# Performance work log

Measured on AMD Instinct MI355X. Metric: run time of the kernel, lower is better.

Reference implementation:

```python
import jax, jax.numpy as jnp
import numpy as np

L, B, T, C, H, V = 8, 8, 1024, 768, 12, 1024
D = C // H  # head dim 64
FF = 4 * C
EPS = 1e-5


def _ln(h, g, b):
    mu = jnp.mean(h, axis=-1, keepdims=True)
    var = jnp.mean((h - mu) ** 2, axis=-1, keepdims=True)
    return (h - mu) * jax.lax.rsqrt(var + EPS) * g + b


def _ffn(h, W1, b1, W2, b2):
    return jax.nn.gelu(h @ W1 + b1, approximate=False) @ W2 + b2


def setup_inputs() -> dict:
    key = jax.random.key(0)
    ks = jax.random.split(key, 16)
    s = 0.02
    inp = {
        "x": jax.random.randint(ks[0], (B, T), 0, V),
        "embed": jax.random.normal(ks[1], (V, C), jnp.float32) * s,
        "pos": jax.random.normal(ks[2], (T, C), jnp.float32) * s,
        "Wqkv": jax.random.normal(ks[3], (L, C, 3 * C), jnp.float32) * s,
        "bqkv": jnp.zeros((L, 3 * C), jnp.float32),
        "W1a": jax.random.normal(ks[4], (L, C, FF), jnp.float32) * s,
        "b1a": jnp.zeros((L, FF), jnp.float32),
        "W2a": jax.random.normal(ks[5], (L, FF, C), jnp.float32) * s,
        "b2a": jnp.zeros((L, C), jnp.float32),
        "g1": jnp.ones((L, C), jnp.float32),
        "beta1": jnp.zeros((L, C), jnp.float32),
        "W1b": jax.random.normal(ks[6], (L, C, FF), jnp.float32) * s,
        "b1b": jnp.zeros((L, FF), jnp.float32),
        "W2b": jax.random.normal(ks[7], (L, FF, C), jnp.float32) * s,
        "b2b": jnp.zeros((L, C), jnp.float32),
        "g2": jnp.ones((L, C), jnp.float32),
        "beta2": jnp.zeros((L, C), jnp.float32),
        "lm_W": jax.random.normal(ks[8], (C, V), jnp.float32) * s,
        "lm_b": jnp.zeros((V,), jnp.float32),
    }
    return inp


def reference(x, embed, pos, Wqkv, bqkv, W1a, b1a, W2a, b2a, g1, beta1,
              W1b, b1b, W2b, b2b, g2, beta2, lm_W, lm_b):
    h = embed[x] + pos[:T]  # (B,T,C)
    causal = jnp.tril(jnp.ones((T, T), bool))

    def block(h, p):
        (Wqkv, bqkv, W1a, b1a, W2a, b2a, g1, beta1,
         W1b, b1b, W2b, b2b, g2, beta2) = p
        qkv = h @ Wqkv + bqkv  # (B,T,3C); split order is K,Q,V per source
        K, Q, Vv = jnp.split(qkv, 3, axis=-1)
        K = K.reshape(B, T, H, D).transpose(0, 2, 1, 3)
        Q = Q.reshape(B, T, H, D).transpose(0, 2, 1, 3)
        Vv = Vv.reshape(B, T, H, D).transpose(0, 2, 1, 3)
        att = jnp.einsum("bhqd,bhkd->bhqk", Q, K) / jnp.sqrt(jnp.float32(D))
        att = jnp.where(causal, att, -jnp.inf)
        att = jax.nn.softmax(att, axis=-1)
        y = jnp.einsum("bhqk,bhkd->bhqd", att, Vv)
        y = y.transpose(0, 2, 1, 3).reshape(B, T, C)
        y = _ffn(y, W1a, b1a, W2a, b2a)  # FFN inside SelfAttn
        h = h + _ln(y, g1, beta1)        # post-norm residual, as in source
        h = h + _ln(_ffn(h, W1b, b1b, W2b, b2b), g2, beta2)
        return h, None

    params = (Wqkv, bqkv, W1a, b1a, W2a, b2a, g1, beta1,
              W1b, b1b, W2b, b2b, g2, beta2)
    h, _ = jax.lax.scan(block, h, params)
    return h @ lm_W + lm_b  # (B,T,V) logits
```

## Files before the change

### kernel.cpp

```cpp
#include <hip/hip_runtime.h>
#include <hip/hip_bf16.h>

#define L_ 8
#define B_ 8
#define T_ 1024
#define C_ 768
#define H_ 12
#define D_HEAD 64
#define V_ 1024
#define FF_ 3072
#define M_ (B_ * T_)

typedef __bf16 bf16x8 __attribute__((ext_vector_type(8)));
typedef float f32x4 __attribute__((ext_vector_type(4)));

typedef const __attribute__((address_space(1))) void* as1cvp;
typedef __attribute__((address_space(3))) void* as3vp;

__device__ __forceinline__ void async16(const void* g, void* l) {
  __builtin_amdgcn_global_load_lds((as1cvp)g, (as3vp)l, 16, 0, 0);
}

__device__ __forceinline__ float bf2f(unsigned short u) {
  union { unsigned u32; float f; } c; c.u32 = ((unsigned)u) << 16; return c.f;
}

__device__ __forceinline__ unsigned short f2bf(float f) {
  __hip_bfloat16 h = __float2bfloat16(f);
  return *(unsigned short*)&h;
}

__device__ __forceinline__ float gelu_f(float x) {
  return 0.5f * x * (1.0f + erff(x * 0.70710678118654752f));
}

__global__ __launch_bounds__(256) void embed_kernel(
    const int* __restrict__ x, const float* __restrict__ emb,
    const float* __restrict__ pos, float* __restrict__ h,
    __hip_bfloat16* __restrict__ hb) {
  int row = blockIdx.x;
  int t = row & (T_ - 1);
  int id = x[row];
#pragma unroll
  for (int j = 0; j < 3; ++j) {
    int c = threadIdx.x + j * 256;
    float v = emb[(size_t)id * C_ + c] + pos[(size_t)t * C_ + c];
    h[(size_t)row * C_ + c] = v;
    hb[(size_t)row * C_ + c] = __float2bfloat16(v);
  }
}

__global__ void transpose_cast(const float* __restrict__ W,
                               __hip_bfloat16* __restrict__ Wt, int K, int N) {
  __shared__ float tile[32][33];
  int nb = blockIdx.x * 32, kb = blockIdx.y * 32;
  int tx = threadIdx.x, ty = threadIdx.y;
#pragma unroll
  for (int r = 0; r < 4; ++r)
    tile[ty + r * 8][tx] = W[(size_t)(kb + ty + r * 8) * N + nb + tx];
  __syncthreads();
#pragma unroll
  for (int r = 0; r < 4; ++r)
    Wt[(size_t)(nb + ty + r * 8) * K + kb + tx] =
        __float2bfloat16(tile[tx][ty + r * 8]);
}

__global__ void transpose_cast2(const float* __restrict__ Wa,
                                __hip_bfloat16* __restrict__ Wta,
                                const float* __restrict__ Wb,
                                __hip_bfloat16* __restrict__ Wtb, int K, int N) {
  __shared__ float tile[32][33];
  const float* W = blockIdx.z ? Wb : Wa;
  __hip_bfloat16* Wt = blockIdx.z ? Wtb : Wta;
  int nb = blockIdx.x * 32, kb = blockIdx.y * 32;
  int tx = threadIdx.x, ty = threadIdx.y;
#pragma unroll
  for (int r = 0; r < 4; ++r)
    tile[ty + r * 8][tx] = W[(size_t)(kb + ty + r * 8) * N + nb + tx];
  __syncthreads();
#pragma unroll
  for (int r = 0; r < 4; ++r)
    Wt[(size_t)(nb + ty + r * 8) * K + kb + tx] =
        __float2bfloat16(tile[tx][ty + r * 8]);
}

template <int ACT_GELU, int OUT_BF16>
__global__ __launch_bounds__(256, 2) void gemm_bt(
    const __hip_bfloat16* __restrict__ A, const __hip_bfloat16* __restrict__ Bt,
    const float* __restrict__ bias, void* __restrict__ Cv, int M, int N, int K) {
  __shared__ __align__(16) __hip_bfloat16 As[128 * 32];
  __shared__ __align__(16) __hip_bfloat16 Bs[128 * 32];
  const int tid = threadIdx.x;
  const int lane = tid & 63, wv = tid >> 6;
  const int lane4 = lane & 15, quad = lane >> 4;
  const int wr = wv >> 1, wc = wv & 1;
  const int bm = blockIdx.y * 128, bn = blockIdx.x * 128;

  const int r0 = tid >> 2, kc0 = (tid & 3) * 8;
  const __hip_bfloat16* gA0 = A + (size_t)(bm + r0) * K + kc0;
  const __hip_bfloat16* gA1 = gA0 + (size_t)64 * K;
  const __hip_bfloat16* gB0 = Bt + (size_t)(bn + r0) * K + kc0;
  const __hip_bfloat16* gB1 = gB0 + (size_t)64 * K;
  __hip_bfloat16* lA0 = As + tid * 8;
  __hip_bfloat16* lA1 = As + (tid + 256) * 8;
  __hip_bfloat16* lB0 = Bs + tid * 8;
  __hip_bfloat16* lB1 = Bs + (tid + 256) * 8;

  f32x4 acc[4][4] = {};

  for (int k0 = 0; k0 < K; k0 += 32) {
    async16(gA0 + k0, lA0);
    async16(gA1 + k0, lA1);
    async16(gB0 + k0, lB0);
    async16(gB1 + k0, lB1);
    __syncthreads();
    bf16x8 af[4], bfv[4];
#pragma unroll
    for (int i = 0; i < 4; ++i)
      af[i] = *(const bf16x8*)(As + (wr * 64 + i * 16 + lane4) * 32 + quad * 8);
#pragma unroll
    for (int j = 0; j < 4; ++j)
      bfv[j] = *(const bf16x8*)(Bs + (wc * 64 + j * 16 + lane4) * 32 + quad * 8);
#pragma unroll
    for (int i = 0; i < 4; ++i)
#pragma unroll
      for (int j = 0; j < 4; ++j)
        acc[i][j] = __builtin_amdgcn_mfma_f32_16x16x32_bf16(af[i], bfv[j],
                                                            acc[i][j], 0, 0, 0);
    __syncthreads();
  }

#pragma unroll
  for (int i = 0; i < 4; ++i) {
    int row0 = bm + wr * 64 + i * 16 + quad * 4;
#pragma unroll
    for (int j = 0; j < 4; ++j) {
      int col = bn + wc * 64 + j * 16 + lane4;
      float bv = bias[col];
#pragma unroll
      for (int r = 0; r < 4; ++r) {
        float v = acc[i][j][r] + bv;
        if (ACT_GELU) v = gelu_f(v);
        size_t off = (size_t)(row0 + r) * N + col;
        if (OUT_BF16)
          ((__hip_bfloat16*)Cv)[off] = __float2bfloat16(v);
        else
          ((float*)Cv)[off] = v;
      }
    }
  }
}

__global__ __launch_bounds__(256) void attn_mfma(
    const __hip_bfloat16* __restrict__ qkv, __hip_bfloat16* __restrict__ y) {
  __shared__ __align__(16) __hip_bfloat16 VtS[64][72];
  __shared__ __align__(16) __hip_bfloat16 Ps[4][16][72];

  const int tid = threadIdx.x;
  const int lane = tid & 63, w = tid >> 6;
  const int lane4 = lane & 15, quad = lane >> 4;
  const int qt = gridDim.x - 1 - blockIdx.x;
  const int bh = blockIdx.y;
  const int b = bh / H_, hh = bh % H_;
  const unsigned short* qk16 = (const unsigned short*)qkv;
  const size_t base = (size_t)b * T_ * (3 * C_) + hh * D_HEAD;

  union FragU { bf16x8 v; unsigned short s[8]; uint4 q; };

  FragU aq[2];
  {
    const unsigned short* qp =
        qk16 + base + (size_t)(qt * 64 + w * 16 + lane4) * (3 * C_) + C_ +
        quad * 8;
#pragma unroll
    for (int c = 0; c < 2; ++c) {
      FragU t;
      t.q = *(const uint4*)(qp + c * 32);
#pragma unroll
      for (int j = 0; j < 8; ++j) aq[c].s[j] = f2bf(bf2f(t.s[j]) * 0.125f);
    }
  }

  const unsigned short* kbase0 =
      qk16 + base + (size_t)(lane4)*(3 * C_) + quad * 8;
  const unsigned short* vbase =
      qk16 + base + (size_t)lane * (3 * C_) + 2 * C_ + w * 16;
  const size_t tile_stride = (size_t)64 * (3 * C_);

  f32x4 o_acc[4] = {};
  float m_r[4] = {-1e30f, -1e30f, -1e30f, -1e30f};
  float l_r[4] = {0.f, 0.f, 0.f, 0.f};

  FragU kc[4][2];
  uint4 vc0, vc1;
  {
    const unsigned short* kp = kbase0;
#pragma unroll
    for (int nt = 0; nt < 4; ++nt) {
      kc[nt][0].q = *(const uint4*)(kp + nt * 16 * (3 * C_));
      kc[nt][1].q = *(const uint4*)(kp + nt * 16 * (3 * C_) + 32);
    }
    vc0 = *(const uint4*)vbase;
    vc1 = *(const uint4*)(vbase + 8);
  }

  for (int kt = 0; kt <= qt; ++kt) {
    FragU kn[4][2];
    uint4 vn0, vn1;
    {
      int ktn = (kt < qt) ? kt + 1 : qt;
      const unsigned short* kp = kbase0 + (size_t)ktn * tile_stride;
#pragma unroll
      for (int nt = 0; nt < 4; ++nt) {
        kn[nt][0].q = *(const uint4*)(kp + nt * 16 * (3 * C_));
        kn[nt][1].q = *(const uint4*)(kp + nt * 16 * (3 * C_) + 32);
      }
      const unsigned short* vp = vbase + (size_t)ktn * tile_stride;
      vn0 = *(const uint4*)vp;
      vn1 = *(const uint4*)(vp + 8);
    }

    f32x4 s_acc[4] = {};
#pragma unroll
    for (int nt = 0; nt < 4; ++nt) {
      s_acc[nt] = __builtin_amdgcn_mfma_f32_16x16x32_bf16(aq[0].v, kc[nt][0].v,
                                                          s_acc[nt], 0, 0, 0);
      s_acc[nt] = __builtin_amdgcn_mfma_f32_16x16x32_bf16(aq[1].v, kc[nt][1].v,
                                                          s_acc[nt], 0, 0, 0);
    }

    if (kt == qt) {
      int qloc = w * 16 + quad * 4;
#pragma unroll
      for (int nt = 0; nt < 4; ++nt) {
        int kloc = nt * 16 + lane4;
#pragma unroll
        for (int r = 0; r < 4; ++r)
          if (kloc > qloc + r) s_acc[nt][r] = -1e30f;
      }
    }

    float p[4][4], alpha[4], ts[4];
#pragma unroll
    for (int r = 0; r < 4; ++r) {
      float tm = fmaxf(fmaxf(s_acc[0][r], s_acc[1][r]),
                       fmaxf(s_acc[2][r], s_acc[3][r]));
      tm = fmaxf(tm, __shfl_xor(tm, 1));
      tm = fmaxf(tm, __shfl_xor(tm, 2));
      tm = fmaxf(tm, __shfl_xor(tm, 4));
      tm = fmaxf(tm, __shfl_xor(tm, 8));
      float mn = fmaxf(m_r[r], tm);
      alpha[r] = __expf(m_r[r] - mn);
      m_r[r] = mn;
      float sr = 0.f;
#pragma unroll
      for (int nt = 0; nt < 4; ++nt) {
        float pv = __expf(s_acc[nt][r] - mn);
        p[nt][r] = pv;
        sr += pv;
      }
      sr += __shfl_xor(sr, 1);
      sr += __shfl_xor(sr, 2);
      sr += __shfl_xor(sr, 4);
      sr += __shfl_xor(sr, 8);
      ts[r] = sr;
    }
#pragma unroll
    for (int r = 0; r < 4; ++r) {
      l_r[r] = l_r[r] * alpha[r] + ts[r];
#pragma unroll
      for (int nt = 0; nt < 4; ++nt) o_acc[nt][r] *= alpha[r];
    }

    __syncthreads();

    {
      const unsigned short* vs = (const unsigned short*)&vc0;
#pragma unroll
      for (int j = 0; j < 8; ++j)
        *(unsigned short*)&VtS[w * 16 + j][lane] = vs[j];
      vs = (const unsigned short*)&vc1;
#pragma unroll
      for (int j = 0; j < 8; ++j)
        *(unsigned short*)&VtS[w * 16 + 8 + j][lane] = vs[j];
    }
#pragma unroll
    for (int nt = 0; nt < 4; ++nt)
#pragma unroll
      for (int r = 0; r < 4; ++r)
        *(unsigned short*)&Ps[w][quad * 4 + r][nt * 16 + lane4] =
            f2bf(p[nt][r]);

    __syncthreads();

    FragU ap0, ap1;
    ap0.v = *(const bf16x8*)&Ps[w][lane4][quad * 8];
    ap1.v = *(const bf16x8*)&Ps[w][lane4][32 + quad * 8];
#pragma unroll
    for (int nt = 0; nt < 4; ++nt) {
      bf16x8 bv0 = *(const bf16x8*)&VtS[nt * 16 + lane4][quad * 8];
      bf16x8 bv1 = *(const bf16x8*)&VtS[nt * 16 + lane4][32 + quad * 8];
      o_acc[nt] = __builtin_amdgcn_mfma_f32_16x16x32_bf16(ap0.v, bv0,
                                                          o_acc[nt], 0, 0, 0);
      o_acc[nt] = __builtin_amdgcn_mfma_f32_16x16x32_bf16(ap1.v, bv1,
                                                          o_acc[nt], 0, 0, 0);
    }

#pragma unroll
    for (int nt = 0; nt < 4; ++nt) {
      kc[nt][0] = kn[nt][0];
      kc[nt][1] = kn[nt][1];
    }
    vc0 = vn0;
    vc1 = vn1;
  }

  float inv[4];
#pragma unroll
  for (int r = 0; r < 4; ++r) inv[r] = 1.f / l_r[r];
#pragma unroll
  for (int nt = 0; nt < 4; ++nt) {
#pragma unroll
    for (int r = 0; r < 4; ++r) {
      int row = qt * 64 + w * 16 + quad * 4 + r;
      __hip_bfloat16* yp =
          y + (size_t)(b * T_ + row) * C_ + hh * D_HEAD + nt * 16 + lane4;
      *yp = __float2bfloat16(o_acc[nt][r] * inv[r]);
    }
  }
}

__global__ __launch_bounds__(256) void resid_ln(
    float* __restrict__ h, const float* __restrict__ z,
    const float* __restrict__ g, const float* __restrict__ be,
    __hip_bfloat16* __restrict__ hb) {
  int row = blockIdx.x;
  int tid = threadIdx.x;
  const float* zr = z + (size_t)row * C_;
  float v[3], s = 0.f, s2 = 0.f;
#pragma unroll
  for (int j = 0; j < 3; ++j) {
    v[j] = zr[tid + 256 * j];
    s += v[j];
    s2 += v[j] * v[j];
  }
#pragma unroll
  for (int msk = 1; msk < 64; msk <<= 1) {
    s += __shfl_xor(s, msk);
    s2 += __shfl_xor(s2, msk);
  }
  __shared__ float red[8];
  int w = tid >> 6;
  if ((tid & 63) == 0) { red[w] = s; red[4 + w] = s2; }
  __syncthreads();
  s = red[0] + red[1] + red[2] + red[3];
  s2 = red[4] + red[5] + red[6] + red[7];
  float mu = s * (1.f / C_);
  float var = s2 * (1.f / C_) - mu * mu;
  float rstd = rsqrtf(var + 1e-5f);
  float* hr = h + (size_t)row * C_;
  __hip_bfloat16* hbr = hb + (size_t)row * C_;
#pragma unroll
  for (int j = 0; j < 3; ++j) {
    int c = tid + 256 * j;
    float nv = hr[c] + (v[j] - mu) * rstd * g[c] + be[c];
    hr[c] = nv;
    hbr[c] = __float2bfloat16(nv);
  }
}

extern "C" void kernel_launch(void* const* d_in, const int* in_sizes, int n_in,
                              void* d_out, int out_size, void* d_ws,
                              size_t ws_size, hipStream_t stream) {
  const int* x = (const int*)d_in[0];
  const float* embed = (const float*)d_in[1];
  const float* pos = (const float*)d_in[2];
  const float* Wqkv = (const float*)d_in[3];
  const float* bqkv = (const float*)d_in[4];
  const float* W1a = (const float*)d_in[5];
  const float* b1a = (const float*)d_in[6];
  const float* W2a = (const float*)d_in[7];
  const float* b2a = (const float*)d_in[8];
  const float* g1 = (const float*)d_in[9];
  const float* be1 = (const float*)d_in[10];
  const float* W1b = (const float*)d_in[11];
  const float* b1b = (const float*)d_in[12];
  const float* W2b = (const float*)d_in[13];
  const float* b2b = (const float*)d_in[14];
  const float* g2 = (const float*)d_in[15];
  const float* be2 = (const float*)d_in[16];
  const float* lmW = (const float*)d_in[17];
  const float* lmb = (const float*)d_in[18];
  float* out = (float*)d_out;

  char* p = (char*)d_ws;
  auto alloc = [&](size_t bytes) {
    void* r = (void*)p;
    p += (bytes + 255) & ~(size_t)255;
    return r;
  };
  float* h = (float*)alloc((size_t)M_ * C_ * 4);
  __hip_bfloat16* hb = (__hip_bfloat16*)alloc((size_t)M_ * C_ * 2);
  __hip_bfloat16* qkv = (__hip_bfloat16*)alloc((size_t)M_ * 3 * C_ * 2);
  __hip_bfloat16* ybuf = (__hip_bfloat16*)alloc((size_t)M_ * C_ * 2);
  __hip_bfloat16* ubuf = (__hip_bfloat16*)alloc((size_t)M_ * FF_ * 2);
  float* zbuf = (float*)alloc((size_t)M_ * C_ * 4);
  __hip_bfloat16* Wtqkv = (__hip_bfloat16*)alloc((size_t)(3 * C_) * C_ * 2);
  __hip_bfloat16* Wt1a = (__hip_bfloat16*)alloc((size_t)FF_ * C_ * 2);
  __hip_bfloat16* Wt1b = (__hip_bfloat16*)alloc((size_t)FF_ * C_ * 2);
  __hip_bfloat16* Wt2a = (__hip_bfloat16*)alloc((size_t)C_ * FF_ * 2);
  __hip_bfloat16* Wt2b = (__hip_bfloat16*)alloc((size_t)C_ * FF_ * 2);

  dim3 blk256(256);
  embed_kernel<<<M_, blk256, 0, stream>>>(x, embed, pos, h, hb);

  for (int l = 0; l < L_; ++l) {
    transpose_cast<<<dim3(3 * C_ / 32, C_ / 32), dim3(32, 8), 0, stream>>>(
        Wqkv + (size_t)l * C_ * 3 * C_, Wtqkv, C_, 3 * C_);
    transpose_cast2<<<dim3(FF_ / 32, C_ / 32, 2), dim3(32, 8), 0, stream>>>(
        W1a + (size_t)l * C_ * FF_, Wt1a, W1b + (size_t)l * C_ * FF_, Wt1b,
        C_, FF_);
    transpose_cast2<<<dim3(C_ / 32, FF_ / 32, 2), dim3(32, 8), 0, stream>>>(
        W2a + (size_t)l * FF_ * C_, Wt2a, W2b + (size_t)l * FF_ * C_, Wt2b,
        FF_, C_);

    gemm_bt<0, 1><<<dim3(3 * C_ / 128, M_ / 128), blk256, 0, stream>>>(
        hb, Wtqkv, bqkv + (size_t)l * 3 * C_, qkv, M_, 3 * C_, C_);
    attn_mfma<<<dim3(T_ / 64, B_ * H_), blk256, 0, stream>>>(qkv, ybuf);
    gemm_bt<1, 1><<<dim3(FF_ / 128, M_ / 128), blk256, 0, stream>>>(
        ybuf, Wt1a, b1a + (size_t)l * FF_, ubuf, M_, FF_, C_);
    gemm_bt<0, 0><<<dim3(C_ / 128, M_ / 128), blk256, 0, stream>>>(
        ubuf, Wt2a, b2a + (size_t)l * C_, zbuf, M_, C_, FF_);
    resid_ln<<<M_, blk256, 0, stream>>>(h, zbuf, g1 + (size_t)l * C_,
                                        be1 + (size_t)l * C_, hb);
    gemm_bt<1, 1><<<dim3(FF_ / 128, M_ / 128), blk256, 0, stream>>>(
        hb, Wt1b, b1b + (size_t)l * FF_, ubuf, M_, FF_, C_);
    gemm_bt<0, 0><<<dim3(C_ / 128, M_ / 128), blk256, 0, stream>>>(
        ubuf, Wt2b, b2b + (size_t)l * C_, zbuf, M_, C_, FF_);
    resid_ln<<<M_, blk256, 0, stream>>>(h, zbuf, g2 + (size_t)l * C_,
                                        be2 + (size_t)l * C_, hb);
  }

  transpose_cast<<<dim3(V_ / 32, C_ / 32), dim3(32, 8), 0, stream>>>(
      lmW, Wtqkv, C_, V_);
  gemm_bt<0, 0><<<dim3(V_ / 128, M_ / 128), blk256, 0, stream>>>(
      hb, Wtqkv, lmb, out, M_, V_, C_);
}
```

Before: 4.149 ms.

## Pair causal attention query tiles per block and transpose MFMA operands

```diff
diff --git a/kernel.cpp b/kernel.cpp
--- a/kernel.cpp
+++ b/kernel.cpp
@@ -153,179 +153,182 @@
 
 __global__ __launch_bounds__(256) void attn_mfma(
     const __hip_bfloat16* __restrict__ qkv, __hip_bfloat16* __restrict__ y) {
-  __shared__ __align__(16) __hip_bfloat16 VtS[64][72];
-  __shared__ __align__(16) __hip_bfloat16 Ps[4][16][72];
+  __shared__ __align__(16) __hip_bfloat16 VtS[2][64][72];
+  __shared__ __align__(16) __hip_bfloat16 Ps[2][4][16][72];
 
   const int tid = threadIdx.x;
   const int lane = tid & 63, w = tid >> 6;
   const int lane4 = lane & 15, quad = lane >> 4;
-  const int qt = gridDim.x - 1 - blockIdx.x;
   const int bh = blockIdx.y;
   const int b = bh / H_, hh = bh % H_;
   const unsigned short* qk16 = (const unsigned short*)qkv;
   const size_t base = (size_t)b * T_ * (3 * C_) + hh * D_HEAD;
+  const size_t tile_stride = (size_t)64 * (3 * C_);
+  const int NTILE = T_ / 64;
 
   union FragU { bf16x8 v; unsigned short s[8]; uint4 q; };
 
-  FragU aq[2];
-  {
-    const unsigned short* qp =
-        qk16 + base + (size_t)(qt * 64 + w * 16 + lane4) * (3 * C_) + C_ +
-        quad * 8;
-#pragma unroll
-    for (int c = 0; c < 2; ++c) {
-      FragU t;
-      t.q = *(const uint4*)(qp + c * 32);
-#pragma unroll
-      for (int j = 0; j < 8; ++j) aq[c].s[j] = f2bf(bf2f(t.s[j]) * 0.125f);
-    }
-  }
-
   const unsigned short* kbase0 =
-      qk16 + base + (size_t)(lane4)*(3 * C_) + quad * 8;
+      qk16 + base + (size_t)lane4 * (3 * C_) + quad * 8;
   const unsigned short* vbase =
       qk16 + base + (size_t)lane * (3 * C_) + 2 * C_ + w * 16;
-  const size_t tile_stride = (size_t)64 * (3 * C_);
-
-  f32x4 o_acc[4] = {};
-  float m_r[4] = {-1e30f, -1e30f, -1e30f, -1e30f};
-  float l_r[4] = {0.f, 0.f, 0.f, 0.f};
-
-  FragU kc[4][2];
-  uint4 vc0, vc1;
-  {
-    const unsigned short* kp = kbase0;
-#pragma unroll
-    for (int nt = 0; nt < 4; ++nt) {
-      kc[nt][0].q = *(const uint4*)(kp + nt * 16 * (3 * C_));
-      kc[nt][1].q = *(const uint4*)(kp + nt * 16 * (3 * C_) + 32);
+
+  int buf = 0;
+
+  for (int qi = 0; qi < 2; ++qi) {
+    const int qt = qi ? blockIdx.x : (NTILE - 1 - blockIdx.x);
+
+    FragU aq[2];
+    {
+      const unsigned short* qp =
+          qk16 + base + (size_t)(qt * 64 + w * 16 + lane4) * (3 * C_) + C_ +
+          quad * 8;
+#pragma unroll
+      for (int c = 0; c < 2; ++c) {
+        FragU t;
+        t.q = *(const uint4*)(qp + c * 32);
+#pragma unroll
+        for (int j = 0; j < 8; ++j) aq[c].s[j] = f2bf(bf2f(t.s[j]) * 0.125f);
+      }
     }
-    vc0 = *(const uint4*)vbase;
-    vc1 = *(const uint4*)(vbase + 8);
-  }
-
-  for (int kt = 0; kt <= qt; ++kt) {
-    FragU kn[4][2];
-    uint4 vn0, vn1;
+
+    f32x4 o_acc[4] = {};
+    float m_r = -1e30f, l_r = 0.f;
+
+    FragU kc[4][2];
+    uint4 vc0, vc1;
     {
-      int ktn = (kt < qt) ? kt + 1 : qt;
-      const unsigned short* kp = kbase0 + (size_t)ktn * tile_stride;
+      const unsigned short* kp = kbase0;
 #pragma unroll
       for (int nt = 0; nt < 4; ++nt) {
-        kn[nt][0].q = *(const uint4*)(kp + nt * 16 * (3 * C_));
-        kn[nt][1].q = *(const uint4*)(kp + nt * 16 * (3 * C_) + 32);
-      }
-      const unsigned short* vp = vbase + (size_t)ktn * tile_stride;
-      vn0 = *(const uint4*)vp;
-      vn1 = *(const uint4*)(vp + 8);
+        kc[nt][0].q = *(const uint4*)(kp + nt * 16 * (3 * C_));
+        kc[nt][1].q = *(const uint4*)(kp + nt * 16 * (3 * C_) + 32);
+      }
+      vc0 = *(const uint4*)vbase;
+      vc1 = *(const uint4*)(vbase + 8);
     }
 
-    f32x4 s_acc[4] = {};
-#pragma unroll
-    for (int nt = 0; nt < 4; ++nt) {
-      s_acc[nt] = __builtin_amdgcn_mfma_f32_16x16x32_bf16(aq[0].v, kc[nt][0].v,
-                                                          s_acc[nt], 0, 0, 0);
-      s_acc[nt] = __builtin_amdgcn_mfma_f32_16x16x32_bf16(aq[1].v, kc[nt][1].v,
-                                                          s_acc[nt], 0, 0, 0);
+    for (int kt = 0; kt <= qt; ++kt) {
+      FragU kn[4][2];
+      uint4 vn0, vn1;
+      {
+        int ktn = (kt < qt) ? kt + 1 : qt;
+        const unsigned short* kp = kbase0 + (size_t)ktn * tile_stride;
+#pragma unroll
+        for (int nt = 0; nt < 4; ++nt) {
+          kn[nt][0].q = *(const uint4*)(kp + nt * 16 * (3 * C_));
+          kn[nt][1].q = *(const uint4*)(kp + nt * 16 * (3 * C_) + 32);
+        }
+        const unsigned short* vp = vbase + (size_t)ktn * tile_stride;
+        vn0 = *(const uint4*)vp;
+        vn1 = *(const uint4*)(vp + 8);
+      }
+
+      f32x4 s_acc[4] = {};
+#pragma unroll
+      for (int nt = 0; nt < 4; ++nt) {
+        s_acc[nt] = __builtin_amdgcn_mfma_f32_16x16x32_bf16(
+            kc[nt][0].v, aq[0].v, s_acc[nt], 0, 0, 0);
+        s_acc[nt] = __builtin_amdgcn_mfma_f32_16x16x32_bf16(
+            kc[nt][1].v, aq[1].v, s_acc[nt], 0, 0, 0);
+      }
+
+      if (kt == qt) {
+        int qloc = w * 16 + lane4;
+#pragma unroll
+        for (int nt = 0; nt < 4; ++nt) {
+          int k0loc = nt * 16 + quad * 4;
+#pragma unroll
+          for (int r = 0; r < 4; ++r)
+            if (k0loc + r > qloc) s_acc[nt][r] = -1e30f;
+        }
+      }
+
+      float a0 = fmaxf(fmaxf(s_acc[0][0], s_acc[0][1]),
+                       fmaxf(s_acc[0][2], s_acc[0][3]));
+      float a1 = fmaxf(fmaxf(s_acc[1][0], s_acc[1][1]),
+                       fmaxf(s_acc[1][2], s_acc[1][3]));
+      float a2 = fmaxf(fmaxf(s_acc[2][0], s_acc[2][1]),
+                       fmaxf(s_acc[2][2], s_acc[2][3]));
+      float a3 = fmaxf(fmaxf(s_acc[3][0], s_acc[3][1]),
+                       fmaxf(s_acc[3][2], s_acc[3][3]));
+      float tm = fmaxf(fmaxf(a0, a1), fmaxf(a2, a3));
+      tm = fmaxf(tm, __shfl_xor(tm, 16));
+      tm = fmaxf(tm, __shfl_xor(tm, 32));
+      float mn = fmaxf(m_r, tm);
+      float alpha = __expf(m_r - mn);
+      m_r = mn;
+
+      float sr = 0.f;
+#pragma unroll
+      for (int nt = 0; nt < 4; ++nt) {
+        float p0 = __expf(s_acc[nt][0] - mn);
+        float p1 = __expf(s_acc[nt][1] - mn);
+        float p2 = __expf(s_acc[nt][2] - mn);
+        float p3 = __expf(s_acc[nt][3] - mn);
+        sr += (p0 + p1) + (p2 + p3);
+        union { unsigned short s[4]; uint2 u; } pk;
+        pk.s[0] = f2bf(p0);
+        pk.s[1] = f2bf(p1);
+        pk.s[2] = f2bf(p2);
+        pk.s[3] = f2bf(p3);
+        *(uint2*)&Ps[buf][w][lane4][nt * 16 + quad * 4] = pk.u;
+      }
+      sr += __shfl_xor(sr, 16);
+      sr += __shfl_xor(sr, 32);
+      l_r = l_r * alpha + sr;
+
+#pragma unroll
+      for (int dt = 0; dt < 4; ++dt)
+#pragma unroll
+        for (int r = 0; r < 4; ++r) o_acc[dt][r] *= alpha;
+
+      {
+        const unsigned short* vs = (const unsigned short*)&vc0;
+#pragma unroll
+        for (int j = 0; j < 8; ++j)
+          *(unsigned short*)&VtS[buf][w * 16 + j][lane] = vs[j];
+        vs = (const unsigned short*)&vc1;
+#pragma unroll
+        for (int j = 0; j < 8; ++j)
+          *(unsigned short*)&VtS[buf][w * 16 + 8 + j][lane] = vs[j];
+      }
+
+      __syncthreads();
+
+      FragU pp0, pp1;
+      pp0.v = *(const bf16x8*)&Ps[buf][w][lane4][quad * 8];
+      pp1.v = *(const bf16x8*)&Ps[buf][w][lane4][32 + quad * 8];
+#pragma unroll
+      for (int dt = 0; dt < 4; ++dt) {
+        bf16x8 bv0 = *(const bf16x8*)&VtS[buf][dt * 16 + lane4][quad * 8];
+        bf16x8 bv1 = *(const bf16x8*)&VtS[buf][dt * 16 + lane4][32 + quad * 8];
+        o_acc[dt] = __builtin_amdgcn_mfma_f32_16x16x32_bf16(bv0, pp0.v,
+                                                            o_acc[dt], 0, 0, 0);
+        o_acc[dt] = __builtin_amdgcn_mfma_f32_16x16x32_bf16(bv1, pp1.v,
+                                                            o_acc[dt], 0, 0, 0);
+      }
+
+#pragma unroll
+      for (int nt = 0; nt < 4; ++nt) {
+        kc[nt][0] = kn[nt][0];
+        kc[nt][1] = kn[nt][1];
+      }
+      vc0 = vn0;
+      vc1 = vn1;
+      buf ^= 1;
     }
 
-    if (kt == qt) {
-      int qloc = w * 16 + quad * 4;
-#pragma unroll
-      for (int nt = 0; nt < 4; ++nt) {
-        int kloc = nt * 16 + lane4;
-#pragma unroll
-        for (int r = 0; r < 4; ++r)
-          if (kloc > qloc + r) s_acc[nt][r] = -1e30f;
-      }
-    }
-
-    float p[4][4], alpha[4], ts[4];
-#pragma unroll
-    for (int r = 0; r < 4; ++r) {
-      float tm = fmaxf(fmaxf(s_acc[0][r], s_acc[1][r]),
-                       fmaxf(s_acc[2][r], s_acc[3][r]));
-      tm = fmaxf(tm, __shfl_xor(tm, 1));
-      tm = fmaxf(tm, __shfl_xor(tm, 2));
-      tm = fmaxf(tm, __shfl_xor(tm, 4));
-      tm = fmaxf(tm, __shfl_xor(tm, 8));
-      float mn = fmaxf(m_r[r], tm);
-      alpha[r] = __expf(m_r[r] - mn);
-      m_r[r] = mn;
-      float sr = 0.f;
-#pragma unroll
-      for (int nt = 0; nt < 4; ++nt) {
-        float pv = __expf(s_acc[nt][r] - mn);
-        p[nt][r] = pv;
-        sr += pv;
-      }
-      sr += __shfl_xor(sr, 1);
-      sr += __shfl_xor(sr, 2);
-      sr += __shfl_xor(sr, 4);
-      sr += __shfl_xor(sr, 8);
-      ts[r] = sr;
-    }
-#pragma unroll
-    for (int r = 0; r < 4; ++r) {
-      l_r[r] = l_r[r] * alpha[r] + ts[r];
-#pragma unroll
-      for (int nt = 0; nt < 4; ++nt) o_acc[nt][r] *= alpha[r];
-    }
-
-    __syncthreads();
-
-    {
-      const unsigned short* vs = (const unsigned short*)&vc0;
-#pragma unroll
-      for (int j = 0; j < 8; ++j)
-        *(unsigned short*)&VtS[w * 16 + j][lane] = vs[j];
-      vs = (const unsigned short*)&vc1;
-#pragma unroll
-      for (int j = 0; j < 8; ++j)
-        *(unsigned short*)&VtS[w * 16 + 8 + j][lane] = vs[j];
-    }
-#pragma unroll
-    for (int nt = 0; nt < 4; ++nt)
-#pragma unroll
-      for (int r = 0; r < 4; ++r)
-        *(unsigned short*)&Ps[w][quad * 4 + r][nt * 16 + lane4] =
-            f2bf(p[nt][r]);
-
-    __syncthreads();
-
-    FragU ap0, ap1;
-    ap0.v = *(const bf16x8*)&Ps[w][lane4][quad * 8];
-    ap1.v = *(const bf16x8*)&Ps[w][lane4][32 + quad * 8];
-#pragma unroll
-    for (int nt = 0; nt < 4; ++nt) {
-      bf16x8 bv0 = *(const bf16x8*)&VtS[nt * 16 + lane4][quad * 8];
-      bf16x8 bv1 = *(const bf16x8*)&VtS[nt * 16 + lane4][32 + quad * 8];
-      o_acc[nt] = __builtin_amdgcn_mfma_f32_16x16x32_bf16(ap0.v, bv0,
-                                                          o_acc[nt], 0, 0, 0);
-      o_acc[nt] = __builtin_amdgcn_mfma_f32_16x16x32_bf16(ap1.v, bv1,
-                                                          o_acc[nt], 0, 0, 0);
-    }
-
-#pragma unroll
-    for (int nt = 0; nt < 4; ++nt) {
-      kc[nt][0] = kn[nt][0];
-      kc[nt][1] = kn[nt][1];
-    }
-    vc0 = vn0;
-    vc1 = vn1;
-  }
-
-  float inv[4];
-#pragma unroll
-  for (int r = 0; r < 4; ++r) inv[r] = 1.f / l_r[r];
-#pragma unroll
-  for (int nt = 0; nt < 4; ++nt) {
-#pragma unroll
-    for (int r = 0; r < 4; ++r) {
-      int row = qt * 64 + w * 16 + quad * 4 + r;
-      __hip_bfloat16* yp =
-          y + (size_t)(b * T_ + row) * C_ + hh * D_HEAD + nt * 16 + lane4;
-      *yp = __float2bfloat16(o_acc[nt][r] * inv[r]);
+    float invl = 1.f / l_r;
+    int qrow = qt * 64 + w * 16 + lane4;
+    unsigned short* yp =
+        (unsigned short*)y + (size_t)(b * T_ + qrow) * C_ + hh * D_HEAD;
+#pragma unroll
+    for (int dt = 0; dt < 4; ++dt) {
+      union { unsigned short s[4]; uint2 u; } ok;
+#pragma unroll
+      for (int r = 0; r < 4; ++r) ok.s[r] = f2bf(o_acc[dt][r] * invl);
+      *(uint2*)(yp + dt * 16 + quad * 4) = ok.u;
     }
   }
 }
@@ -426,7 +429,7 @@
 
     gemm_bt<0, 1><<<dim3(3 * C_ / 128, M_ / 128), blk256, 0, stream>>>(
         hb, Wtqkv, bqkv + (size_t)l * 3 * C_, qkv, M_, 3 * C_, C_);
-    attn_mfma<<<dim3(T_ / 64, B_ * H_), blk256, 0, stream>>>(qkv, ybuf);
+    attn_mfma<<<dim3(T_ / 128, B_ * H_), blk256, 0, stream>>>(qkv, ybuf);
     gemm_bt<1, 1><<<dim3(FF_ / 128, M_ / 128), blk256, 0, stream>>>(
         ybuf, Wt1a, b1a + (size_t)l * FF_, ubuf, M_, FF_, C_);
     gemm_bt<0, 0><<<dim3(C_ / 128, M_ / 128), blk256, 0, stream>>>(
```

Measured after the change: 3.733 ms. 1.11x faster.
